# Optimization experiments

Hardware: AMD Instinct MI355X
Metric: run time of the kernel (lower is better)

## Reference

```python
import jax, jax.numpy as jnp
import numpy as np

DIM = 192
RC = 16
M = 64
LN_EPS = 1e-5
NORM_EPS = 1e-12


def _layernorm(x, g, b):
    mu = jnp.mean(x, axis=-1, keepdims=True)
    var = jnp.mean((x - mu) ** 2, axis=-1, keepdims=True)
    return (x - mu) / jnp.sqrt(var + LN_EPS) * g + b


def _l2norm(x):
    n = jnp.sqrt(jnp.sum(x * x, axis=-1, keepdims=True))
    return x / jnp.maximum(n, NORM_EPS)


def setup_inputs() -> dict:
    key = jax.random.key(0)
    ks = jax.random.split(key, 12)
    B, N = 8, 16384
    s_q = 1.0 / np.sqrt(DIM)
    inp = {
        "x": jax.random.normal(ks[0], (B, N, DIM), jnp.float32),
        "dict_tokens": jax.random.normal(ks[1], (B, M, DIM), jnp.float32),
        "H": 128,
        "W": 128,
        "wq_w": jax.random.normal(ks[2], (DIM, RC), jnp.float32) * s_q,
        "wq_b": jnp.zeros((RC,), jnp.float32),
        "wk_w": jax.random.normal(ks[3], (DIM, RC), jnp.float32) * s_q,
        "wk_b": jnp.zeros((RC,), jnp.float32),
        "wv_w": jax.random.normal(ks[4], (DIM, DIM), jnp.float32) * s_q,
        "wv_b": jnp.zeros((DIM,), jnp.float32),
        "qn_g": jnp.ones((RC,), jnp.float32),
        "qn_b": jnp.zeros((RC,), jnp.float32),
        "kn_g": jnp.ones((RC,), jnp.float32),
        "kn_b": jnp.zeros((RC,), jnp.float32),
        "conv_w": jax.random.normal(ks[5], (DIM, 1, 3, 3), jnp.float32) / 3.0,
        "conv_b": jnp.zeros((DIM,), jnp.float32),
        "temperature": jnp.ones((1,), jnp.float32),
    }
    return inp


def reference(x, dict_tokens, H, W, wq_w, wq_b, wk_w, wk_b, wv_w, wv_b,
              qn_g, qn_b, kn_g, kn_b, conv_w, conv_b, temperature):
    # q: (B,N,rc), k: (B,M,rc)
    q = _l2norm(_layernorm(x @ wq_w + wq_b, qn_g, qn_b))
    k = _l2norm(_layernorm(dict_tokens @ wk_w + wk_b, kn_g, kn_b))
    # cosine-similarity attention with clamped temperature
    attn = jnp.einsum("bnr,bmr->bnm", q, k) / jnp.maximum(temperature, 0.5)
    attn = jax.nn.softmax(attn, axis=-1)
    # value + depthwise-conv refinement over the M token axis (Mx1 image)
    v = dict_tokens @ wv_w + wv_b                       # (B,M,C)
    v_img = jnp.transpose(v, (0, 2, 1))[..., None]      # (B,C,M,1)
    v_img = jax.lax.conv_general_dilated(
        v_img, conv_w, window_strides=(1, 1), padding=((1, 1), (1, 1)),
        dimension_numbers=("NCHW", "OIHW", "NCHW"), feature_group_count=DIM)
    v_img = v_img + conv_b[None, :, None, None]
    v_img = jax.nn.gelu(v_img, approximate=False)
    v = jnp.transpose(v_img[..., 0], (0, 2, 1))         # (B,M,C)
    out = jnp.einsum("bnm,bmc->bnc", attn, v)           # (B,N,C)
    return out, attn
```

## Files before the change

### kernel.cpp

```cpp
#include <hip/hip_runtime.h>
#include <math.h>

#define B_   8
#define N_   16384
#define M_   64
#define C_   192
#define RC_  16

__global__ __launch_bounds__(256) void k_v_kernel(
    const float* __restrict__ dict, const float* __restrict__ wv_w,
    const float* __restrict__ wv_b, float* __restrict__ ws_v)
{
    const int idx = blockIdx.x * 256 + threadIdx.x;
    const int c   = idx % C_;
    const int row = idx / C_;
    const float* dr = dict + row * C_;
    float acc = wv_b[c];
    #pragma unroll 4
    for (int d = 0; d < C_; ++d)
        acc = fmaf(dr[d], wv_w[d * C_ + c], acc);
    ws_v[idx] = acc;
}

__global__ __launch_bounds__(256) void k_k_kernel(
    const float* __restrict__ dict, const float* __restrict__ wk_w,
    const float* __restrict__ wk_b, const float* __restrict__ kn_g,
    const float* __restrict__ kn_b, float* __restrict__ ws_k)
{
    const int b  = blockIdx.x;
    const int m  = threadIdx.x >> 2;
    const int j4 = threadIdx.x & 3;
    const int c0 = j4 * 4;
    const float* dr = dict + (b * M_ + m) * C_;

    float a0 = wk_b[c0+0], a1 = wk_b[c0+1], a2 = wk_b[c0+2], a3 = wk_b[c0+3];
    #pragma unroll 4
    for (int d4 = 0; d4 < C_/4; ++d4) {
        const float4 xv = ((const float4*)dr)[d4];
        const float4 w0 = *(const float4*)&wk_w[(d4*4+0)*RC_ + c0];
        const float4 w1 = *(const float4*)&wk_w[(d4*4+1)*RC_ + c0];
        const float4 w2 = *(const float4*)&wk_w[(d4*4+2)*RC_ + c0];
        const float4 w3 = *(const float4*)&wk_w[(d4*4+3)*RC_ + c0];
        a0 = fmaf(xv.x, w0.x, a0); a1 = fmaf(xv.x, w0.y, a1); a2 = fmaf(xv.x, w0.z, a2); a3 = fmaf(xv.x, w0.w, a3);
        a0 = fmaf(xv.y, w1.x, a0); a1 = fmaf(xv.y, w1.y, a1); a2 = fmaf(xv.y, w1.z, a2); a3 = fmaf(xv.y, w1.w, a3);
        a0 = fmaf(xv.z, w2.x, a0); a1 = fmaf(xv.z, w2.y, a1); a2 = fmaf(xv.z, w2.z, a2); a3 = fmaf(xv.z, w2.w, a3);
        a0 = fmaf(xv.w, w3.x, a0); a1 = fmaf(xv.w, w3.y, a1); a2 = fmaf(xv.w, w3.z, a2); a3 = fmaf(xv.w, w3.w, a3);
    }
    float s  = a0 + a1 + a2 + a3;
    float ss = a0*a0 + a1*a1 + a2*a2 + a3*a3;
    s  += __shfl_xor(s, 1);  s  += __shfl_xor(s, 2);
    ss += __shfl_xor(ss, 1); ss += __shfl_xor(ss, 2);
    const float mu   = s * (1.0f/16.0f);
    const float var  = ss * (1.0f/16.0f) - mu*mu;
    const float rstd = rsqrtf(var + 1e-5f);
    const float4 g4 = *(const float4*)&kn_g[c0];
    const float4 b4 = *(const float4*)&kn_b[c0];
    float y0 = (a0 - mu) * rstd * g4.x + b4.x;
    float y1 = (a1 - mu) * rstd * g4.y + b4.y;
    float y2 = (a2 - mu) * rstd * g4.z + b4.z;
    float y3 = (a3 - mu) * rstd * g4.w + b4.w;
    float n2 = y0*y0 + y1*y1 + y2*y2 + y3*y3;
    n2 += __shfl_xor(n2, 1); n2 += __shfl_xor(n2, 2);
    const float inv = 1.0f / fmaxf(sqrtf(n2), 1e-12f);
    float4 o; o.x = y0*inv; o.y = y1*inv; o.z = y2*inv; o.w = y3*inv;
    *(float4*)&ws_k[(b * M_ + m) * RC_ + c0] = o;
}

__global__ __launch_bounds__(256) void k_conv_kernel(
    const float* __restrict__ ws_v, const float* __restrict__ conv_w,
    const float* __restrict__ conv_b, float* __restrict__ ws_vg)
{
    const int idx = blockIdx.x * 256 + threadIdx.x;
    const int c   = idx % C_;
    const int m   = (idx / C_) % M_;
    const float ctr = ws_v[idx];
    const float up  = (m > 0)      ? ws_v[idx - C_] : 0.0f;
    const float dn  = (m < M_ - 1) ? ws_v[idx + C_] : 0.0f;
    const float w0 = conv_w[c*9 + 1];
    const float w1 = conv_w[c*9 + 4];
    const float w2 = conv_w[c*9 + 7];
    float t = conv_b[c];
    t = fmaf(up, w0, t); t = fmaf(ctr, w1, t); t = fmaf(dn, w2, t);
    ws_vg[idx] = 0.5f * t * (1.0f + erff(t * 0.70710678118654752f));
}

__global__ __launch_bounds__(256, 2) void k_main_kernel(
    const float* __restrict__ x, const float* __restrict__ ws_k,
    const float* __restrict__ ws_vg,
    const float* __restrict__ wq_w, const float* __restrict__ wq_b,
    const float* __restrict__ qn_g, const float* __restrict__ qn_b,
    const float* __restrict__ temp,
    float* __restrict__ out, float* __restrict__ attn_out)
{
    __shared__ float vg_s[M_ * C_];
    __shared__ float attn_s[M_ * 68];
    __shared__ float q_s[M_ * 20];
    __shared__ float k_s[M_ * RC_];

    const int tid = threadIdx.x;
    const int b   = blockIdx.x >> 8;
    const int n0  = (blockIdx.x & 255) * M_;

    {
        const float4* src = (const float4*)(ws_vg + b * (M_ * C_));
        float4*       dst = (float4*)vg_s;
        #pragma unroll
        for (int i = 0; i < 12; ++i)
            dst[tid + 256 * i] = src[tid + 256 * i];
        ((float4*)k_s)[tid] = ((const float4*)(ws_k + b * (M_ * RC_)))[tid];
    }

    const int r  = tid >> 2;
    const int j4 = tid & 3;
    const int c0 = j4 * 4;

    const float* xr = x + (size_t)(b * N_ + n0 + r) * C_;
    float a0 = wq_b[c0+0], a1 = wq_b[c0+1], a2 = wq_b[c0+2], a3 = wq_b[c0+3];
    #pragma unroll 4
    for (int d4 = 0; d4 < C_/4; ++d4) {
        const float4 xv = ((const float4*)xr)[d4];
        const float4 w0 = *(const float4*)&wq_w[(d4*4+0)*RC_ + c0];
        const float4 w1 = *(const float4*)&wq_w[(d4*4+1)*RC_ + c0];
        const float4 w2 = *(const float4*)&wq_w[(d4*4+2)*RC_ + c0];
        const float4 w3 = *(const float4*)&wq_w[(d4*4+3)*RC_ + c0];
        a0 = fmaf(xv.x, w0.x, a0); a1 = fmaf(xv.x, w0.y, a1); a2 = fmaf(xv.x, w0.z, a2); a3 = fmaf(xv.x, w0.w, a3);
        a0 = fmaf(xv.y, w1.x, a0); a1 = fmaf(xv.y, w1.y, a1); a2 = fmaf(xv.y, w1.z, a2); a3 = fmaf(xv.y, w1.w, a3);
        a0 = fmaf(xv.z, w2.x, a0); a1 = fmaf(xv.z, w2.y, a1); a2 = fmaf(xv.z, w2.z, a2); a3 = fmaf(xv.z, w2.w, a3);
        a0 = fmaf(xv.w, w3.x, a0); a1 = fmaf(xv.w, w3.y, a1); a2 = fmaf(xv.w, w3.z, a2); a3 = fmaf(xv.w, w3.w, a3);
    }
    {
        float s  = a0 + a1 + a2 + a3;
        float ss = a0*a0 + a1*a1 + a2*a2 + a3*a3;
        s  += __shfl_xor(s, 1);  s  += __shfl_xor(s, 2);
        ss += __shfl_xor(ss, 1); ss += __shfl_xor(ss, 2);
        const float mu   = s * (1.0f/16.0f);
        const float var  = ss * (1.0f/16.0f) - mu*mu;
        const float rstd = rsqrtf(var + 1e-5f);
        const float4 g4 = *(const float4*)&qn_g[c0];
        const float4 b4 = *(const float4*)&qn_b[c0];
        const float y0 = (a0 - mu) * rstd * g4.x + b4.x;
        const float y1 = (a1 - mu) * rstd * g4.y + b4.y;
        const float y2 = (a2 - mu) * rstd * g4.z + b4.z;
        const float y3 = (a3 - mu) * rstd * g4.w + b4.w;
        float n2 = y0*y0 + y1*y1 + y2*y2 + y3*y3;
        n2 += __shfl_xor(n2, 1); n2 += __shfl_xor(n2, 2);
        const float inv = 1.0f / fmaxf(sqrtf(n2), 1e-12f);
        float4 o; o.x = y0*inv; o.y = y1*inv; o.z = y2*inv; o.w = y3*inv;
        *(float4*)&q_s[r*20 + c0] = o;
    }

    __syncthreads();

    {
        const float tinv = 1.0f / fmaxf(temp[0], 0.5f);
        const float4 q0 = *(const float4*)&q_s[r*20 + 0];
        const float4 q1 = *(const float4*)&q_s[r*20 + 4];
        const float4 q2 = *(const float4*)&q_s[r*20 + 8];
        const float4 q3 = *(const float4*)&q_s[r*20 + 12];
        float sc[16];
        #pragma unroll
        for (int mm = 0; mm < 16; ++mm) {
            const int m = j4*16 + mm;
            const float4 k0 = *(const float4*)&k_s[m*RC_ + 0];
            const float4 k1 = *(const float4*)&k_s[m*RC_ + 4];
            const float4 k2 = *(const float4*)&k_s[m*RC_ + 8];
            const float4 k3 = *(const float4*)&k_s[m*RC_ + 12];
            float d = q0.x*k0.x;
            d = fmaf(q0.y, k0.y, d); d = fmaf(q0.z, k0.z, d); d = fmaf(q0.w, k0.w, d);
            d = fmaf(q1.x, k1.x, d); d = fmaf(q1.y, k1.y, d); d = fmaf(q1.z, k1.z, d); d = fmaf(q1.w, k1.w, d);
            d = fmaf(q2.x, k2.x, d); d = fmaf(q2.y, k2.y, d); d = fmaf(q2.z, k2.z, d); d = fmaf(q2.w, k2.w, d);
            d = fmaf(q3.x, k3.x, d); d = fmaf(q3.y, k3.y, d); d = fmaf(q3.z, k3.z, d); d = fmaf(q3.w, k3.w, d);
            sc[mm] = d * tinv;
        }
        float mx = sc[0];
        #pragma unroll
        for (int mm = 1; mm < 16; ++mm) mx = fmaxf(mx, sc[mm]);
        mx = fmaxf(mx, __shfl_xor(mx, 1)); mx = fmaxf(mx, __shfl_xor(mx, 2));
        float es = 0.0f;
        #pragma unroll
        for (int mm = 0; mm < 16; ++mm) { sc[mm] = expf(sc[mm] - mx); es += sc[mm]; }
        es += __shfl_xor(es, 1); es += __shfl_xor(es, 2);
        const float einv = 1.0f / es;
        float* aw = attn_out + (size_t)(b * N_ + n0 + r) * M_ + j4*16;
        #pragma unroll
        for (int mq = 0; mq < 4; ++mq) {
            float4 av;
            av.x = sc[mq*4+0]*einv; av.y = sc[mq*4+1]*einv;
            av.z = sc[mq*4+2]*einv; av.w = sc[mq*4+3]*einv;
            *(float4*)&attn_s[r*68 + j4*16 + mq*4] = av;
            ((float4*)aw)[mq] = av;
        }
    }

    __syncthreads();

    {
        float4 acc[12];
        #pragma unroll
        for (int cc = 0; cc < 12; ++cc) { acc[cc].x = 0.f; acc[cc].y = 0.f; acc[cc].z = 0.f; acc[cc].w = 0.f; }
        for (int m = 0; m < M_; ++m) {
            const float a = attn_s[r*68 + m];
            #pragma unroll
            for (int cc = 0; cc < 12; ++cc) {
                const float4 v = *(const float4*)&vg_s[m*C_ + cc*16 + c0];
                acc[cc].x = fmaf(a, v.x, acc[cc].x);
                acc[cc].y = fmaf(a, v.y, acc[cc].y);
                acc[cc].z = fmaf(a, v.z, acc[cc].z);
                acc[cc].w = fmaf(a, v.w, acc[cc].w);
            }
        }
        float* orow = out + (size_t)(b * N_ + n0 + r) * C_;
        #pragma unroll
        for (int cc = 0; cc < 12; ++cc)
            *(float4*)&orow[cc*16 + c0] = acc[cc];
    }
}

extern "C" void kernel_launch(void* const* d_in, const int* in_sizes, int n_in,
                              void* d_out, int out_size, void* d_ws, size_t ws_size,
                              hipStream_t stream) {
    const float* x      = (const float*)d_in[0];
    const float* dict   = (const float*)d_in[1];
    const float* wq_w   = (const float*)d_in[4];
    const float* wq_b   = (const float*)d_in[5];
    const float* wk_w   = (const float*)d_in[6];
    const float* wk_b   = (const float*)d_in[7];
    const float* wv_w   = (const float*)d_in[8];
    const float* wv_b   = (const float*)d_in[9];
    const float* qn_g   = (const float*)d_in[10];
    const float* qn_b   = (const float*)d_in[11];
    const float* kn_g   = (const float*)d_in[12];
    const float* kn_b   = (const float*)d_in[13];
    const float* conv_w = (const float*)d_in[14];
    const float* conv_b = (const float*)d_in[15];
    const float* temp   = (const float*)d_in[16];

    float* out  = (float*)d_out;
    float* attn = out + (size_t)B_ * N_ * C_;

    float* ws_v  = (float*)d_ws;
    float* ws_vg = ws_v  + B_ * M_ * C_;
    float* ws_k  = ws_vg + B_ * M_ * C_;

    k_v_kernel   <<<B_ * M_ * C_ / 256, 256, 0, stream>>>(dict, wv_w, wv_b, ws_v);
    k_k_kernel   <<<B_,                 256, 0, stream>>>(dict, wk_w, wk_b, kn_g, kn_b, ws_k);
    k_conv_kernel<<<B_ * M_ * C_ / 256, 256, 0, stream>>>(ws_v, conv_w, conv_b, ws_vg);
    k_main_kernel<<<B_ * (N_ / M_),     256, 0, stream>>>(x, ws_k, ws_vg, wq_w, wq_b,
                                                          qn_g, qn_b, temp, out, attn);
}
```

Baseline: 350.4 us.

## Fuse prep kernels and retile attention-value matmul with register-blocked rows

The three small prologue kernels (V projection, K projection with norms, depthwise conv+GELU) are merged into one per-(batch,token) kernel that recomputes neighbouring V rows instead of round-tripping through workspace. In the main kernel, q is broadcast via lane shuffles instead of shared memory, the global loads of V and K are issued early into registers and stored to LDS after the Q projection, and attention is stored transposed. The attn@V loop is retiled so each thread computes a 4-row by 12-column block, raising reuse per LDS read. The trade-offs are higher register pressure and redundant V FLOPs in the prep kernel, plus scattered scalar attn stores replacing float4 stores.

Measured after the change: 343.9 us. About the same (-1.9%).

```diff
diff --git a/kernel.cpp b/kernel.cpp
--- a/kernel.cpp
+++ b/kernel.cpp
@@ -6,82 +6,82 @@
 #define M_   64
 #define C_   192
 #define RC_  16
-
-__global__ __launch_bounds__(256) void k_v_kernel(
-    const float* __restrict__ dict, const float* __restrict__ wv_w,
-    const float* __restrict__ wv_b, float* __restrict__ ws_v)
+#define AT_S 68
+
+#define FMA4(acc, s, v) \
+    acc.x = fmaf(s, v.x, acc.x); acc.y = fmaf(s, v.y, acc.y); \
+    acc.z = fmaf(s, v.z, acc.z); acc.w = fmaf(s, v.w, acc.w)
+
+__global__ __launch_bounds__(256) void k_prep_kernel(
+    const float* __restrict__ dict,
+    const float* __restrict__ wv_w, const float* __restrict__ wv_b,
+    const float* __restrict__ conv_w, const float* __restrict__ conv_b,
+    const float* __restrict__ wk_w, const float* __restrict__ wk_b,
+    const float* __restrict__ kn_g, const float* __restrict__ kn_b,
+    float* __restrict__ ws_vg, float* __restrict__ ws_k)
 {
-    const int idx = blockIdx.x * 256 + threadIdx.x;
-    const int c   = idx % C_;
-    const int row = idx / C_;
-    const float* dr = dict + row * C_;
-    float acc = wv_b[c];
-    #pragma unroll 4
-    for (int d = 0; d < C_; ++d)
-        acc = fmaf(dr[d], wv_w[d * C_ + c], acc);
-    ws_v[idx] = acc;
-}
-
-__global__ __launch_bounds__(256) void k_k_kernel(
-    const float* __restrict__ dict, const float* __restrict__ wk_w,
-    const float* __restrict__ wk_b, const float* __restrict__ kn_g,
-    const float* __restrict__ kn_b, float* __restrict__ ws_k)
-{
-    const int b  = blockIdx.x;
-    const int m  = threadIdx.x >> 2;
-    const int j4 = threadIdx.x & 3;
-    const int c0 = j4 * 4;
-    const float* dr = dict + (b * M_ + m) * C_;
-
-    float a0 = wk_b[c0+0], a1 = wk_b[c0+1], a2 = wk_b[c0+2], a3 = wk_b[c0+3];
-    #pragma unroll 4
-    for (int d4 = 0; d4 < C_/4; ++d4) {
-        const float4 xv = ((const float4*)dr)[d4];
-        const float4 w0 = *(const float4*)&wk_w[(d4*4+0)*RC_ + c0];
-        const float4 w1 = *(const float4*)&wk_w[(d4*4+1)*RC_ + c0];
-        const float4 w2 = *(const float4*)&wk_w[(d4*4+2)*RC_ + c0];
-        const float4 w3 = *(const float4*)&wk_w[(d4*4+3)*RC_ + c0];
-        a0 = fmaf(xv.x, w0.x, a0); a1 = fmaf(xv.x, w0.y, a1); a2 = fmaf(xv.x, w0.z, a2); a3 = fmaf(xv.x, w0.w, a3);
-        a0 = fmaf(xv.y, w1.x, a0); a1 = fmaf(xv.y, w1.y, a1); a2 = fmaf(xv.y, w1.z, a2); a3 = fmaf(xv.y, w1.w, a3);
-        a0 = fmaf(xv.z, w2.x, a0); a1 = fmaf(xv.z, w2.y, a1); a2 = fmaf(xv.z, w2.z, a2); a3 = fmaf(xv.z, w2.w, a3);
-        a0 = fmaf(xv.w, w3.x, a0); a1 = fmaf(xv.w, w3.y, a1); a2 = fmaf(xv.w, w3.z, a2); a3 = fmaf(xv.w, w3.w, a3);
-    }
-    float s  = a0 + a1 + a2 + a3;
-    float ss = a0*a0 + a1*a1 + a2*a2 + a3*a3;
-    s  += __shfl_xor(s, 1);  s  += __shfl_xor(s, 2);
-    ss += __shfl_xor(ss, 1); ss += __shfl_xor(ss, 2);
-    const float mu   = s * (1.0f/16.0f);
-    const float var  = ss * (1.0f/16.0f) - mu*mu;
-    const float rstd = rsqrtf(var + 1e-5f);
-    const float4 g4 = *(const float4*)&kn_g[c0];
-    const float4 b4 = *(const float4*)&kn_b[c0];
-    float y0 = (a0 - mu) * rstd * g4.x + b4.x;
-    float y1 = (a1 - mu) * rstd * g4.y + b4.y;
-    float y2 = (a2 - mu) * rstd * g4.z + b4.z;
-    float y3 = (a3 - mu) * rstd * g4.w + b4.w;
-    float n2 = y0*y0 + y1*y1 + y2*y2 + y3*y3;
-    n2 += __shfl_xor(n2, 1); n2 += __shfl_xor(n2, 2);
-    const float inv = 1.0f / fmaxf(sqrtf(n2), 1e-12f);
-    float4 o; o.x = y0*inv; o.y = y1*inv; o.z = y2*inv; o.w = y3*inv;
-    *(float4*)&ws_k[(b * M_ + m) * RC_ + c0] = o;
-}
-
-__global__ __launch_bounds__(256) void k_conv_kernel(
-    const float* __restrict__ ws_v, const float* __restrict__ conv_w,
-    const float* __restrict__ conv_b, float* __restrict__ ws_vg)
-{
-    const int idx = blockIdx.x * 256 + threadIdx.x;
-    const int c   = idx % C_;
-    const int m   = (idx / C_) % M_;
-    const float ctr = ws_v[idx];
-    const float up  = (m > 0)      ? ws_v[idx - C_] : 0.0f;
-    const float dn  = (m < M_ - 1) ? ws_v[idx + C_] : 0.0f;
-    const float w0 = conv_w[c*9 + 1];
-    const float w1 = conv_w[c*9 + 4];
-    const float w2 = conv_w[c*9 + 7];
-    float t = conv_b[c];
-    t = fmaf(up, w0, t); t = fmaf(ctr, w1, t); t = fmaf(dn, w2, t);
-    ws_vg[idx] = 0.5f * t * (1.0f + erff(t * 0.70710678118654752f));
+    const int b   = blockIdx.x >> 6;
+    const int m   = blockIdx.x & 63;
+    const int tid = threadIdx.x;
+    const float* d0 = dict + (b * M_ + m) * C_;
+
+    if (tid < 192) {
+        const int c = tid;
+        const bool hm = (m > 0), hp = (m < M_ - 1);
+        const float* dm = hm ? d0 - C_ : d0;
+        const float* dp = hp ? d0 + C_ : d0;
+        float am = 0.f, ac = 0.f, ap = 0.f;
+        #pragma unroll 4
+        for (int d = 0; d < C_; ++d) {
+            const float w = wv_w[d * C_ + c];
+            am = fmaf(dm[d], w, am);
+            ac = fmaf(d0[d], w, ac);
+            ap = fmaf(dp[d], w, ap);
+        }
+        const float bia = wv_b[c];
+        const float up = hm ? (am + bia) : 0.f;
+        const float ct = ac + bia;
+        const float dn = hp ? (ap + bia) : 0.f;
+        float t = conv_b[c];
+        t = fmaf(up, conv_w[c*9 + 1], t);
+        t = fmaf(ct, conv_w[c*9 + 4], t);
+        t = fmaf(dn, conv_w[c*9 + 7], t);
+        ws_vg[(b * M_ + m) * C_ + c] = 0.5f * t * (1.0f + erff(t * 0.70710678118654752f));
+    } else if (tid < 196) {
+        const int j4 = tid - 192;
+        const int c0 = j4 * 4;
+        float a0 = wk_b[c0+0], a1 = wk_b[c0+1], a2 = wk_b[c0+2], a3 = wk_b[c0+3];
+        #pragma unroll 4
+        for (int d4 = 0; d4 < C_/4; ++d4) {
+            const float4 xv = ((const float4*)d0)[d4];
+            const float4 w0 = *(const float4*)&wk_w[(d4*4+0)*RC_ + c0];
+            const float4 w1 = *(const float4*)&wk_w[(d4*4+1)*RC_ + c0];
+            const float4 w2 = *(const float4*)&wk_w[(d4*4+2)*RC_ + c0];
+            const float4 w3 = *(const float4*)&wk_w[(d4*4+3)*RC_ + c0];
+            a0 = fmaf(xv.x, w0.x, a0); a1 = fmaf(xv.x, w0.y, a1); a2 = fmaf(xv.x, w0.z, a2); a3 = fmaf(xv.x, w0.w, a3);
+            a0 = fmaf(xv.y, w1.x, a0); a1 = fmaf(xv.y, w1.y, a1); a2 = fmaf(xv.y, w1.z, a2); a3 = fmaf(xv.y, w1.w, a3);
+            a0 = fmaf(xv.z, w2.x, a0); a1 = fmaf(xv.z, w2.y, a1); a2 = fmaf(xv.z, w2.z, a2); a3 = fmaf(xv.z, w2.w, a3);
+            a0 = fmaf(xv.w, w3.x, a0); a1 = fmaf(xv.w, w3.y, a1); a2 = fmaf(xv.w, w3.z, a2); a3 = fmaf(xv.w, w3.w, a3);
+        }
+        float s  = a0 + a1 + a2 + a3;
+        float ss = a0*a0 + a1*a1 + a2*a2 + a3*a3;
+        s  += __shfl_xor(s, 1);  s  += __shfl_xor(s, 2);
+        ss += __shfl_xor(ss, 1); ss += __shfl_xor(ss, 2);
+        const float mu   = s * (1.0f/16.0f);
+        const float var  = ss * (1.0f/16.0f) - mu*mu;
+        const float rstd = rsqrtf(var + 1e-5f);
+        const float4 g4 = *(const float4*)&kn_g[c0];
+        const float4 b4 = *(const float4*)&kn_b[c0];
+        const float y0 = (a0 - mu) * rstd * g4.x + b4.x;
+        const float y1 = (a1 - mu) * rstd * g4.y + b4.y;
+        const float y2 = (a2 - mu) * rstd * g4.z + b4.z;
+        const float y3 = (a3 - mu) * rstd * g4.w + b4.w;
+        float n2 = y0*y0 + y1*y1 + y2*y2 + y3*y3;
+        n2 += __shfl_xor(n2, 1); n2 += __shfl_xor(n2, 2);
+        const float inv = 1.0f / fmaxf(sqrtf(n2), 1e-12f);
+        float4 o; o.x = y0*inv; o.y = y1*inv; o.z = y2*inv; o.w = y3*inv;
+        *(float4*)&ws_k[(b * M_ + m) * RC_ + c0] = o;
+    }
 }
 
 __global__ __launch_bounds__(256, 2) void k_main_kernel(
@@ -93,21 +93,21 @@
     float* __restrict__ out, float* __restrict__ attn_out)
 {
     __shared__ float vg_s[M_ * C_];
-    __shared__ float attn_s[M_ * 68];
-    __shared__ float q_s[M_ * 20];
     __shared__ float k_s[M_ * RC_];
-
-    const int tid = threadIdx.x;
-    const int b   = blockIdx.x >> 8;
-    const int n0  = (blockIdx.x & 255) * M_;
-
-    {
-        const float4* src = (const float4*)(ws_vg + b * (M_ * C_));
-        float4*       dst = (float4*)vg_s;
-        #pragma unroll
-        for (int i = 0; i < 12; ++i)
-            dst[tid + 256 * i] = src[tid + 256 * i];
-        ((float4*)k_s)[tid] = ((const float4*)(ws_k + b * (M_ * RC_)))[tid];
+    __shared__ float attn_t[M_ * AT_S];
+
+    const int tid   = threadIdx.x;
+    const int b     = blockIdx.x >> 8;
+    const int n0    = (blockIdx.x & 255) * M_;
+    const int lane  = tid & 63;
+    const int lbase = lane & ~3;
+
+    float4 st[12]; float4 kst;
+    {
+        const float4* vgb4 = (const float4*)(ws_vg + b * (M_ * C_));
+        #pragma unroll
+        for (int i = 0; i < 12; ++i) st[i] = vgb4[tid + 256 * i];
+        kst = ((const float4*)(ws_k + b * (M_ * RC_)))[tid];
     }
 
     const int r  = tid >> 2;
@@ -128,6 +128,7 @@
         a0 = fmaf(xv.z, w2.x, a0); a1 = fmaf(xv.z, w2.y, a1); a2 = fmaf(xv.z, w2.z, a2); a3 = fmaf(xv.z, w2.w, a3);
         a0 = fmaf(xv.w, w3.x, a0); a1 = fmaf(xv.w, w3.y, a1); a2 = fmaf(xv.w, w3.z, a2); a3 = fmaf(xv.w, w3.w, a3);
     }
+    float4 q[4];
     {
         float s  = a0 + a1 + a2 + a3;
         float ss = a0*a0 + a1*a1 + a2*a2 + a3*a3;
@@ -146,30 +147,37 @@
         n2 += __shfl_xor(n2, 1); n2 += __shfl_xor(n2, 2);
         const float inv = 1.0f / fmaxf(sqrtf(n2), 1e-12f);
         float4 o; o.x = y0*inv; o.y = y1*inv; o.z = y2*inv; o.w = y3*inv;
-        *(float4*)&q_s[r*20 + c0] = o;
-    }
-
+        #pragma unroll
+        for (int j = 0; j < 4; ++j) {
+            q[j].x = __shfl(o.x, lbase + j);
+            q[j].y = __shfl(o.y, lbase + j);
+            q[j].z = __shfl(o.z, lbase + j);
+            q[j].w = __shfl(o.w, lbase + j);
+        }
+    }
+    const float tinv = 1.0f / fmaxf(temp[0], 0.5f);
+
+    {
+        #pragma unroll
+        for (int i = 0; i < 12; ++i) ((float4*)vg_s)[tid + 256 * i] = st[i];
+        ((float4*)k_s)[tid] = kst;
+    }
     __syncthreads();
 
     {
-        const float tinv = 1.0f / fmaxf(temp[0], 0.5f);
-        const float4 q0 = *(const float4*)&q_s[r*20 + 0];
-        const float4 q1 = *(const float4*)&q_s[r*20 + 4];
-        const float4 q2 = *(const float4*)&q_s[r*20 + 8];
-        const float4 q3 = *(const float4*)&q_s[r*20 + 12];
         float sc[16];
         #pragma unroll
         for (int mm = 0; mm < 16; ++mm) {
-            const int m = j4*16 + mm;
+            const int m = mm*4 + j4;
             const float4 k0 = *(const float4*)&k_s[m*RC_ + 0];
             const float4 k1 = *(const float4*)&k_s[m*RC_ + 4];
             const float4 k2 = *(const float4*)&k_s[m*RC_ + 8];
             const float4 k3 = *(const float4*)&k_s[m*RC_ + 12];
-            float d = q0.x*k0.x;
-            d = fmaf(q0.y, k0.y, d); d = fmaf(q0.z, k0.z, d); d = fmaf(q0.w, k0.w, d);
-            d = fmaf(q1.x, k1.x, d); d = fmaf(q1.y, k1.y, d); d = fmaf(q1.z, k1.z, d); d = fmaf(q1.w, k1.w, d);
-            d = fmaf(q2.x, k2.x, d); d = fmaf(q2.y, k2.y, d); d = fmaf(q2.z, k2.z, d); d = fmaf(q2.w, k2.w, d);
-            d = fmaf(q3.x, k3.x, d); d = fmaf(q3.y, k3.y, d); d = fmaf(q3.z, k3.z, d); d = fmaf(q3.w, k3.w, d);
+            float d = q[0].x*k0.x;
+            d = fmaf(q[0].y, k0.y, d); d = fmaf(q[0].z, k0.z, d); d = fmaf(q[0].w, k0.w, d);
+            d = fmaf(q[1].x, k1.x, d); d = fmaf(q[1].y, k1.y, d); d = fmaf(q[1].z, k1.z, d); d = fmaf(q[1].w, k1.w, d);
+            d = fmaf(q[2].x, k2.x, d); d = fmaf(q[2].y, k2.y, d); d = fmaf(q[2].z, k2.z, d); d = fmaf(q[2].w, k2.w, d);
+            d = fmaf(q[3].x, k3.x, d); d = fmaf(q[3].y, k3.y, d); d = fmaf(q[3].z, k3.z, d); d = fmaf(q[3].w, k3.w, d);
             sc[mm] = d * tinv;
         }
         float mx = sc[0];
@@ -181,38 +189,48 @@
         for (int mm = 0; mm < 16; ++mm) { sc[mm] = expf(sc[mm] - mx); es += sc[mm]; }
         es += __shfl_xor(es, 1); es += __shfl_xor(es, 2);
         const float einv = 1.0f / es;
-        float* aw = attn_out + (size_t)(b * N_ + n0 + r) * M_ + j4*16;
-        #pragma unroll
-        for (int mq = 0; mq < 4; ++mq) {
-            float4 av;
-            av.x = sc[mq*4+0]*einv; av.y = sc[mq*4+1]*einv;
-            av.z = sc[mq*4+2]*einv; av.w = sc[mq*4+3]*einv;
-            *(float4*)&attn_s[r*68 + j4*16 + mq*4] = av;
-            ((float4*)aw)[mq] = av;
-        }
-    }
-
+        float* aw = attn_out + (size_t)(b * N_ + n0 + r) * M_;
+        #pragma unroll
+        for (int mm = 0; mm < 16; ++mm) {
+            const float p = sc[mm] * einv;
+            attn_t[(mm*4 + j4)*AT_S + r] = p;
+            aw[mm*4 + j4] = p;
+        }
+    }
     __syncthreads();
 
     {
-        float4 acc[12];
-        #pragma unroll
-        for (int cc = 0; cc < 12; ++cc) { acc[cc].x = 0.f; acc[cc].y = 0.f; acc[cc].z = 0.f; acc[cc].w = 0.f; }
+        const int rq = tid >> 4;
+        const int cq = tid & 15;
+        float4 ac0[3], ac1[3], ac2[3], ac3[3];
+        #pragma unroll
+        for (int t = 0; t < 3; ++t) {
+            ac0[t] = make_float4(0.f,0.f,0.f,0.f);
+            ac1[t] = make_float4(0.f,0.f,0.f,0.f);
+            ac2[t] = make_float4(0.f,0.f,0.f,0.f);
+            ac3[t] = make_float4(0.f,0.f,0.f,0.f);
+        }
+        #pragma unroll 4
         for (int m = 0; m < M_; ++m) {
-            const float a = attn_s[r*68 + m];
+            const float4 av = *(const float4*)&attn_t[m*AT_S + rq*4];
+            const float4* vr = (const float4*)(vg_s + m*C_ + cq*12);
             #pragma unroll
-            for (int cc = 0; cc < 12; ++cc) {
-                const float4 v = *(const float4*)&vg_s[m*C_ + cc*16 + c0];
-                acc[cc].x = fmaf(a, v.x, acc[cc].x);
-                acc[cc].y = fmaf(a, v.y, acc[cc].y);
-                acc[cc].z = fmaf(a, v.z, acc[cc].z);
-                acc[cc].w = fmaf(a, v.w, acc[cc].w);
+            for (int t = 0; t < 3; ++t) {
+                const float4 v = vr[t];
+                FMA4(ac0[t], av.x, v);
+                FMA4(ac1[t], av.y, v);
+                FMA4(ac2[t], av.z, v);
+                FMA4(ac3[t], av.w, v);
             }
         }
-        float* orow = out + (size_t)(b * N_ + n0 + r) * C_;
-        #pragma unroll
-        for (int cc = 0; cc < 12; ++cc)
-            *(float4*)&orow[cc*16 + c0] = acc[cc];
+        float* o0 = out + (size_t)(b * N_ + n0 + rq*4) * C_ + cq*12;
+        #pragma unroll
+        for (int t = 0; t < 3; ++t) {
+            *(float4*)&o0[t*4]          = ac0[t];
+            *(float4*)&o0[C_   + t*4]   = ac1[t];
+            *(float4*)&o0[2*C_ + t*4]   = ac2[t];
+            *(float4*)&o0[3*C_ + t*4]   = ac3[t];
+        }
     }
 }
 
@@ -238,13 +256,11 @@
     float* out  = (float*)d_out;
     float* attn = out + (size_t)B_ * N_ * C_;
 
-    float* ws_v  = (float*)d_ws;
-    float* ws_vg = ws_v  + B_ * M_ * C_;
+    float* ws_vg = (float*)d_ws;
     float* ws_k  = ws_vg + B_ * M_ * C_;
 
-    k_v_kernel   <<<B_ * M_ * C_ / 256, 256, 0, stream>>>(dict, wv_w, wv_b, ws_v);
-    k_k_kernel   <<<B_,                 256, 0, stream>>>(dict, wk_w, wk_b, kn_g, kn_b, ws_k);
-    k_conv_kernel<<<B_ * M_ * C_ / 256, 256, 0, stream>>>(ws_v, conv_w, conv_b, ws_vg);
-    k_main_kernel<<<B_ * (N_ / M_),     256, 0, stream>>>(x, ws_k, ws_vg, wq_w, wq_b,
-                                                          qn_g, qn_b, temp, out, attn);
+    k_prep_kernel<<<B_ * M_,        256, 0, stream>>>(dict, wv_w, wv_b, conv_w, conv_b,
+                                                      wk_w, wk_b, kn_g, kn_b, ws_vg, ws_k);
+    k_main_kernel<<<B_ * (N_ / M_), 256, 0, stream>>>(x, ws_k, ws_vg, wq_w, wq_b,
+                                                      qn_g, qn_b, temp, out, attn);
 }
```
